# Performance work log

Hardware: AMD Instinct MI355X
Metric: run time of the kernel (lower is better)

Reference implementation:

```python
import jax, jax.numpy as jnp
import numpy as np

SW, SH = 240.0, 180.0  # sensor size from LIFSpikePool(..., (240, 180))
EPS = 1e-5


def _grid_edges(gw, gh):
    # static 8-neighbor (king-move) grid graph + self loops, src -> dst
    idx = np.arange(gw * gh).reshape(gh, gw)
    srcs, dsts = [], []
    for dy in (-1, 0, 1):
        for dx in (-1, 0, 1):
            s = idx[max(0, dy):gh - max(0, -dy), max(0, dx):gw - max(0, -dx)]
            d = idx[max(0, -dy):gh - max(0, dy), max(0, -dx):gw - max(0, dx)]
            srcs.append(s.reshape(-1)); dsts.append(d.reshape(-1))
    return (jnp.asarray(np.concatenate(srcs), jnp.int32),
            jnp.asarray(np.concatenate(dsts), jnp.int32))

_E1 = _grid_edges(80, 60)
_E2 = _grid_edges(40, 30)
_E3 = _grid_edges(20, 15)


def _bn(h):
    # BatchNorm1d with gamma=1, beta=0 (per initialize_weights), batch stats
    return (h - h.mean(0)) / jnp.sqrt(h.var(0) + EPS)


def _pnconv(x, pos2, src, dst, W, b):
    # PointNetConv with single-Linear nn: msg = Lin([x_j, pos_j - pos_i]), max-aggr
    n = x.shape[0]
    msg = jnp.concatenate([x[src], pos2[src] - pos2[dst]], axis=1) @ W + b
    agg = jax.ops.segment_max(msg, dst, num_segments=n)
    return jnp.where(jnp.isfinite(agg), agg, 0.0)  # empty segments -> 0


def _block(x, pos, src, dst, c1w, c1b, c2w, c2b, lw, lb):
    p2 = pos[:, :2]
    skip = _bn(x @ lw + lb)
    h = jax.nn.relu(_bn(_pnconv(x, p2, src, dst, c1w, c1b)))
    h = _bn(_pnconv(h, p2, src, dst, c2w, c2b))
    return jax.nn.relu(h + skip)


def _pool(x, pos, gw, gh, W, b):
    # LIF spike pooling: integrate membrane per grid cell, fire if v > 1
    cx = jnp.clip((pos[:, 0] * gw / SW).astype(jnp.int32), 0, gw - 1)
    cy = jnp.clip((pos[:, 1] * gh / SH).astype(jnp.int32), 0, gh - 1)
    cell = cy * gw + cx
    mem = jax.ops.segment_sum(x, cell, num_segments=gw * gh)
    v = mem @ W + b
    xo = jnp.where(v > 1.0, v, 0.0)
    gx, gy = jnp.meshgrid(jnp.arange(gw), jnp.arange(gh))  # (gh, gw)
    npos = jnp.stack([(gx.reshape(-1) + 0.5) * SW / gw,
                      (gy.reshape(-1) + 0.5) * SH / gh,
                      jnp.zeros(gw * gh)], axis=1).astype(jnp.float32)
    return xo, npos


def _forward(edge_index, x, pos, *p):
    src, dst = edge_index[0], edge_index[1]
    h = _block(x, pos, src, dst, *p[0:6])
    h, pos = _pool(h, pos, 80, 60, p[24], p[25])
    h = _block(h, pos, _E1[0], _E1[1], *p[6:12]); feat0 = h   # (4800, 32)
    h, pos = _pool(h, pos, 40, 30, p[26], p[27])
    h = _block(h, pos, _E2[0], _E2[1], *p[12:18]); feat1 = h  # (1200, 64)
    h, pos = _pool(h, pos, 20, 15, p[28], p[29])
    h = _block(h, pos, _E3[0], _E3[1], *p[18:24]); feat2 = h  # (300, 128)
    return feat0, feat1, feat2


PNAMES = [f"b{i}_{t}" for i in (1, 2, 3, 4) for t in ("c1w", "c1b", "c2w", "c2b", "lw", "lb")] + \
         [f"p{j}_{t}" for j in (1, 2, 3) for t in ("w", "b")]


def setup_inputs() -> dict:
    key = jax.random.key(0)
    ks = jax.random.split(key, 20)
    N, E = 200000, 3200000
    x = jax.random.normal(ks[0], (N, 1), jnp.float32)
    pos = jax.random.uniform(ks[1], (N, 3), jnp.float32) * jnp.array([SW, SH, 1.0], jnp.float32)
    edge_index = jax.random.randint(ks[2], (2, E), 0, N, jnp.int32)
    def lin(k, fi, fo):
        return jax.random.normal(k, (fi, fo), jnp.float32) * np.sqrt(2.0 / fi)
    inp = {"x": x, "pos": pos, "edge_index": edge_index}
    ki = 3
    for i, (ci, co) in enumerate([(1, 16), (16, 32), (32, 64), (64, 128)], start=1):
        inp[f"b{i}_c1w"] = lin(ks[ki], ci + 2, co); ki += 1
        inp[f"b{i}_c1b"] = jnp.zeros((co,), jnp.float32)
        inp[f"b{i}_c2w"] = lin(ks[ki], co + 2, co); ki += 1
        inp[f"b{i}_c2b"] = jnp.zeros((co,), jnp.float32)
        inp[f"b{i}_lw"] = lin(ks[ki], ci, co); ki += 1
        inp[f"b{i}_lb"] = jnp.zeros((co,), jnp.float32)
    for j, ch in [(1, 16), (2, 32), (3, 64)]:
        inp[f"p{j}_w"] = lin(ks[ki], ch, ch); ki += 1
        inp[f"p{j}_b"] = jnp.zeros((ch,), jnp.float32)
    return inp


def reference(x, pos, edge_index,
              b1_c1w, b1_c1b, b1_c2w, b1_c2b, b1_lw, b1_lb,
              b2_c1w, b2_c1b, b2_c2w, b2_c2b, b2_lw, b2_lb,
              b3_c1w, b3_c1b, b3_c2w, b3_c2b, b3_lw, b3_lb,
              b4_c1w, b4_c1b, b4_c2w, b4_c2b, b4_lw, b4_lb,
              p1_w, p1_b, p2_w, p2_b, p3_w, p3_b):
    params = (b1_c1w, b1_c1b, b1_c2w, b1_c2b, b1_lw, b1_lb,
              b2_c1w, b2_c1b, b2_c2w, b2_c2b, b2_lw, b2_lb,
              b3_c1w, b3_c1b, b3_c2w, b3_c2b, b3_lw, b3_lb,
              b4_c1w, b4_c1b, b4_c2w, b4_c2b, b4_lw, b4_lb,
              p1_w, p1_b, p2_w, p2_b, p3_w, p3_b)
    return _forward(edge_index, x, pos, *params)
```

## Files before the change

kernel.cpp:

```cpp
#include <hip/hip_runtime.h>

#define NN 200000
#define NE 3200000
#define NWG 80
#define TT 1024
static constexpr float EPSV = 1e-5f;

__global__ void k_cnt_prep(const int* __restrict__ ei, int* __restrict__ bktCnt,
                           const float* __restrict__ x, const float* __restrict__ pos,
                           float4* __restrict__ feat, float* __restrict__ xstats){
  __shared__ int cnt[256];
  __shared__ float sv[256], sq[256];
  int t = threadIdx.x;
  cnt[t] = 0;
  int i = blockIdx.x*256 + t;
  float xf = 0.f;
  if (i < NN){
    xf = x[i];
    feat[i] = make_float4(xf, pos[3*i], pos[3*i+1], 0.f);
  }
  sv[t] = (i < NN) ? xf : 0.f;
  sq[t] = sv[t]*sv[t];
  __syncthreads();
  int tile = blockIdx.x*4096;
  #pragma unroll
  for (int k = 0; k < 16; ++k){
    int e = tile + k*256 + t;
    if (e < NE) atomicAdd(&cnt[ei[NE+e]>>10], 1);
  }
  for (int o = 128; o > 0; o >>= 1){
    __syncthreads();
    if (t < o){ sv[t]+=sv[t+o]; sq[t]+=sq[t+o]; }
  }
  __syncthreads();
  if (t == 0){ atomicAdd(&xstats[0], sv[0]); atomicAdd(&xstats[1], sq[0]); }
  if (cnt[t]) atomicAdd(&bktCnt[t], cnt[t]);
}

__global__ void k_bktscan(const int* __restrict__ bktCnt, int* __restrict__ bktBase,
                          int* __restrict__ bktCur){
  __shared__ int s[256];
  int t = threadIdx.x;
  int v = bktCnt[t];
  s[t] = v; __syncthreads();
  for (int o = 1; o < 256; o <<= 1){
    int xv = (t >= o) ? s[t-o] : 0;
    __syncthreads(); s[t] += xv; __syncthreads();
  }
  int excl = s[t] - v;
  bktBase[t] = excl;
  bktCur[t]  = excl;
  if (t == 0){ bktBase[256] = NE; }
}

__global__ void k_part1(const int* __restrict__ ei, int* __restrict__ bktCur,
                        int* __restrict__ pairs){
  __shared__ int cnt[256]; __shared__ int base[256]; __shared__ int rank[256];
  int t = threadIdx.x;
  if (t < 256) cnt[t] = 0;
  __syncthreads();
  int tile = blockIdx.x*16384;
  #pragma unroll
  for (int k = 0; k < 16; ++k){
    int e = tile + k*1024 + t;
    if (e < NE) atomicAdd(&cnt[ei[NE+e]>>10], 1);
  }
  __syncthreads();
  if (t < 256){
    base[t] = cnt[t] ? atomicAdd(&bktCur[t], cnt[t]) : 0;
    rank[t] = 0;
  }
  __syncthreads();
  #pragma unroll
  for (int k = 0; k < 16; ++k){
    int e = tile + k*1024 + t;
    if (e < NE){
      int d = ei[NE+e], s = ei[e];
      int b = d >> 10;
      int r = atomicAdd(&rank[b], 1);
      pairs[base[b] + r] = (s<<10) | (d & 1023);
    }
  }
}

__device__ __forceinline__ unsigned fenc(float f){
  unsigned u = __float_as_uint(f);
  return (u >> 31) ? ~u : (u | 0x80000000u);
}
__device__ __forceinline__ float fdec(unsigned k){
  unsigned u = (k >> 31) ? (k ^ 0x80000000u) : ~k;
  return __uint_as_float(u);
}
#define ENC_NI 0x007FFFFFu

__device__ __forceinline__ int aslot(int d, int c){
  return (d << 4) | ((c + (d >> 1)) & 15);
}

__global__ void __launch_bounds__(1024) k_aggA(const int* __restrict__ pairs, const int* __restrict__ bktBase,
    const float4* __restrict__ feat, const float* __restrict__ pos,
    const float* __restrict__ w48, const float* __restrict__ bias,
    float* __restrict__ H, float* __restrict__ st){
  __shared__ unsigned acc[16384];
  const int b = blockIdx.x, t = threadIdx.x;
  for (int i = t; i < 16384; i += 1024) acc[i] = ENC_NI;
  float w0[16], w1[16], w2[16];
  #pragma unroll
  for (int c = 0; c < 16; ++c){ w0[c]=w48[c]; w1[c]=w48[16+c]; w2[c]=w48[32+c]; }
  const int p0 = bktBase[b], p1 = bktBase[b+1];
  __syncthreads();
  for (int j = p0 + t; j < p1; j += 1024){
    int pr = pairs[j];
    float4 f = feat[pr >> 10];
    int d = pr & 1023;
    int gbase = d << 4;
    int rot = (d >> 1) & 15;
    #pragma unroll
    for (int c = 0; c < 16; ++c){
      float m = f.x*w0[c] + f.y*w1[c] + f.z*w2[c];
      atomicMax(&acc[gbase | ((c + rot) & 15)], fenc(m));
    }
  }
  __syncthreads();
  const int base = b << 10;
  const int width = min(1024, NN - base);
  const int c = t & 15;
  const float b_c = bias[c], w1c = w48[16+c], w2c = w48[32+c];
  float ls = 0.f, lq = 0.f;
  for (int i = t; i < width*16; i += 1024){
    int dl = i >> 4, d = base + dl;
    int rot = (dl >> 1) & 15;
    float o = 0.f;
    if (acc[(dl << 4) | rot] != ENC_NI){
      float px = pos[3*d], py = pos[3*d+1];
      o = fdec(acc[(dl << 4) | ((c + rot) & 15)]) + b_c - (px*w1c + py*w2c);
    }
    H[base*16 + i] = o;
    ls += o; lq += o*o;
  }
  __syncthreads();
  float* sv = (float*)acc; float* sq = sv + 1024;
  sv[t] = ls; sq[t] = lq; __syncthreads();
  for (int o2 = 512; o2 >= 16; o2 >>= 1){ if (t < o2){ sv[t]+=sv[t+o2]; sq[t]+=sq[t+o2]; } __syncthreads(); }
  if (t < 16){ atomicAdd(&st[t], sv[t]); atomicAdd(&st[16+t], sq[t]); }
}

__global__ void __launch_bounds__(1024) k_aggB(const int* __restrict__ pairs, const int* __restrict__ bktBase,
    const float4* __restrict__ A4, const float* __restrict__ pos,
    const float* __restrict__ wpos, const float* __restrict__ bias,
    float* __restrict__ H, float* __restrict__ st){
  __shared__ unsigned acc[16384];
  const int b = blockIdx.x, t = threadIdx.x;
  for (int i = t; i < 16384; i += 1024) acc[i] = ENC_NI;
  const int p0 = bktBase[b], p1 = bktBase[b+1];
  __syncthreads();
  for (int j = p0 + t; j < p1; j += 1024){
    int pr = pairs[j];
    int s = pr >> 10;
    int d = pr & 1023;
    int gbase = d << 4;
    int rot = (d >> 1) & 15;
    float4 a0 = A4[s*4+0], a1 = A4[s*4+1], a2 = A4[s*4+2], a3 = A4[s*4+3];
    float av[16] = {a0.x,a0.y,a0.z,a0.w, a1.x,a1.y,a1.z,a1.w,
                    a2.x,a2.y,a2.z,a2.w, a3.x,a3.y,a3.z,a3.w};
    #pragma unroll
    for (int c = 0; c < 16; ++c)
      atomicMax(&acc[gbase | ((c + rot) & 15)], fenc(av[c]));
  }
  __syncthreads();
  const int base = b << 10;
  const int width = min(1024, NN - base);
  const int c = t & 15;
  const float b_c = bias[c], w1c = wpos[c], w2c = wpos[16+c];
  float ls = 0.f, lq = 0.f;
  for (int i = t; i < width*16; i += 1024){
    int dl = i >> 4, d = base + dl;
    int rot = (dl >> 1) & 15;
    float o = 0.f;
    if (acc[(dl << 4) | rot] != ENC_NI){
      float px = pos[3*d], py = pos[3*d+1];
      o = fdec(acc[(dl << 4) | ((c + rot) & 15)]) + b_c - (px*w1c + py*w2c);
    }
    H[base*16 + i] = o;
    ls += o; lq += o*o;
  }
  __syncthreads();
  float* sv = (float*)acc; float* sq = sv + 1024;
  sv[t] = ls; sq[t] = lq; __syncthreads();
  for (int o2 = 512; o2 >= 16; o2 >>= 1){ if (t < o2){ sv[t]+=sv[t+o2]; sq[t]+=sq[t+o2]; } __syncthreads(); }
  if (t < 16){ atomicAdd(&st[t], sv[t]); atomicAdd(&st[16+t], sq[t]); }
}

__global__ void k_prep2(const float* __restrict__ Hraw, const float* __restrict__ st1,
                        const float* __restrict__ pos, const float* __restrict__ w,
                        float4* __restrict__ A4){
  int idx = blockIdx.x*blockDim.x + threadIdx.x;
  if (idx >= NN*4) return;
  int i = idx >> 2, cg = idx & 3;
  const float inv_n = 1.f/(float)NN;
  float acc0 = 0.f, acc1 = 0.f, acc2 = 0.f, acc3 = 0.f;
  #pragma unroll
  for (int k = 0; k < 16; ++k){
    float mk = st1[k]*inv_n;
    float vk = st1[16+k]*inv_n - mk*mk;
    float ik = rsqrtf(vk + EPSV);
    float h = fmaxf((Hraw[i*16+k]-mk)*ik, 0.f);
    acc0 += h*w[k*16 + cg*4 + 0];
    acc1 += h*w[k*16 + cg*4 + 1];
    acc2 += h*w[k*16 + cg*4 + 2];
    acc3 += h*w[k*16 + cg*4 + 3];
  }
  float px = pos[3*i], py = pos[3*i+1];
  int c0 = cg*4;
  acc0 += px*w[256+c0+0] + py*w[272+c0+0];
  acc1 += px*w[256+c0+1] + py*w[272+c0+1];
  acc2 += px*w[256+c0+2] + py*w[272+c0+2];
  acc3 += px*w[256+c0+3] + py*w[272+c0+3];
  A4[idx] = make_float4(acc0, acc1, acc2, acc3);
}

__global__ void k_comb_pool(const float* __restrict__ H, const float* __restrict__ x,
                            const float* __restrict__ pos, const float* __restrict__ lw,
                            const float* __restrict__ st2, const float* __restrict__ xstats,
                            float* __restrict__ mem){
  int idx = blockIdx.x*blockDim.x + threadIdx.x;
  if (idx >= NN*4) return;
  int i = idx >> 2, cg = idx & 3;
  const float inv_n = 1.f/(float)NN;
  float mx = xstats[0]*inv_n, vx = xstats[1]*inv_n - mx*mx;
  float xc = x[i] - mx;
  float px = pos[3*i], py = pos[3*i+1];
  int cx = (int)(px * 80.f / 240.f); cx = min(max(cx,0),79);
  int cy = (int)(py * 60.f / 180.f); cy = min(max(cy,0),59);
  float* mrow = &mem[(cy*80+cx)*16 + cg*4];
  #pragma unroll
  for (int k = 0; k < 4; ++k){
    int c = cg*4 + k;
    float m2 = st2[c]*inv_n, v2 = st2[16+c]*inv_n - m2*m2;
    float i2 = rsqrtf(v2 + EPSV);
    float a = lw[c];
    float sc = a * rsqrtf(a*a*vx + EPSV);
    float v = (H[i*16+c]-m2)*i2 + xc*sc;
    v = fmaxf(v, 0.f);
    atomicAdd(&mrow[k], v);
  }
}

__device__ __forceinline__ void stwt(float* p, float v){
  __hip_atomic_store(p, v, __ATOMIC_RELAXED, __HIP_MEMORY_SCOPE_AGENT);
}
__device__ __forceinline__ float ldwt(const float* p){
  return __hip_atomic_load(p, __ATOMIC_RELAXED, __HIP_MEMORY_SCOPE_AGENT);
}

__device__ __forceinline__ void gridbar(int* bar, int target){
  __syncthreads();
  const int t = threadIdx.x;
  if (blockIdx.x == 0){
    if (t >= 1 && t < NWG){
      while (__hip_atomic_load(bar + 32*t, __ATOMIC_RELAXED, __HIP_MEMORY_SCOPE_AGENT) < target)
        __builtin_amdgcn_s_sleep(1);
    }
    __syncthreads();
    if (t == 0)
      __hip_atomic_store(bar + 2560, target, __ATOMIC_RELAXED, __HIP_MEMORY_SCOPE_AGENT);
  } else {
    if (t == 0){
      __atomic_signal_fence(__ATOMIC_SEQ_CST);
      __builtin_amdgcn_s_waitcnt(0);
      __atomic_signal_fence(__ATOMIC_SEQ_CST);
      __hip_atomic_store(bar + 32*blockIdx.x, target, __ATOMIC_RELAXED, __HIP_MEMORY_SCOPE_AGENT);
      while (__hip_atomic_load(bar + 2560, __ATOMIC_RELAXED, __HIP_MEMORY_SCOPE_AGENT) < target)
        __builtin_amdgcn_s_sleep(2);
    }
    __syncthreads();
  }
}

struct TailP {
  const float *mem1;
  const float *p1w,*p1b,*p2w,*p2b,*p3w,*p3b;
  const float *c1w2,*c1b2,*c2w2,*c2b2,*lw2,*lb2;
  const float *c1w3,*c1b3,*c2w3,*c2b3,*lw3,*lb3;
  const float *c1w4,*c1b4,*c2w4,*c2b4,*lw4,*lb4;
  float *g2p,*g3p;
  float *stB2sk,*stB2c1,*stB2c2,*stB3sk,*stB3c1,*stB3c2,*stB4sk,*stB4c1,*stB4c2;
  float *out;
  int *bar;
};

template<int GW,int GH,int TW,int TH,int K,int C,bool FIRST>
__device__ __forceinline__ void ph_A(float* buf, float* sv, float* sq,
    const float* __restrict__ Gglob, const float* __restrict__ plw, const float* __restrict__ plb,
    const float* __restrict__ c1w, const float* __restrict__ c1b,
    const float* __restrict__ lw, const float* __restrict__ lb,
    float* stH1, float* stSK, float sx, float sy, int tile)
{
  constexpr int W2=TW+4, nR2=W2*(TH+4);
  constexpr int W1=TW+2, nR1=W1*(TH+2);
  constexpr int nT=TW*TH, NTX=GW/TW;
  const int tx0=(tile%NTX)*TW, ty0=(tile/NTX)*TH;
  float* Gl=buf; float* Sl=Gl+nR2*K; float* H1l=Sl+nR2*C; float* SKl=H1l+nR1*C;
  const int t=threadIdx.x;
  if constexpr (FIRST){
    for (int e=t; e<nR2*K; e+=TT){
      int cell=e/K, k=e-cell*K;
      int gx=tx0-2+cell%W2, gy=ty0-2+cell/W2;
      Sl[e] = (gx>=0&&gx<GW&&gy>=0&&gy<GH) ? Gglob[(gy*GW+gx)*K+k] : 0.f;
    }
    __syncthreads();
    for (int e=t; e<nR2*K; e+=TT){
      int cell=e/K, c=e-cell*K;
      float acc=plb[c];
      #pragma unroll
      for (int k=0;k<K;++k) acc += Sl[cell*K+k]*plw[k*K+c];
      Gl[e] = (acc>1.f)?acc:0.f;
    }
  } else {
    for (int e=t; e<nR2*K; e+=TT){
      int cell=e/K, k=e-cell*K;
      int gx=tx0-2+cell%W2, gy=ty0-2+cell/W2;
      Gl[e] = (gx>=0&&gx<GW&&gy>=0&&gy<GH) ? ldwt(&Gglob[(gy*GW+gx)*K+k]) : 0.f;
    }
  }
  __syncthreads();
  for (int e=t; e<nR2*C; e+=TT){
    int cell=e/C, c=e-cell*C;
    float acc=0.f;
    #pragma unroll 8
    for (int k=0;k<K;++k) acc += Gl[cell*K+k]*c1w[k*C+c];
    Sl[e]=acc;
  }
  float ls=0.f,lq=0.f;
  for (int e=t; e<nT*C; e+=TT){
    int cell=e/C, c=e-cell*C;
    int lx=cell%TW, ly=cell/TW;
    int g2=(ly+2)*W2+(lx+2);
    float acc=lb[c];
    #pragma unroll 8
    for (int k=0;k<K;++k) acc += Gl[g2*K+k]*lw[k*C+c];
    SKl[e]=acc; ls+=acc; lq+=acc*acc;
  }
  __syncthreads();
  sv[t]=ls; sq[t]=lq; __syncthreads();
  for (int o=TT/2;o>=C;o>>=1){ if(t<o){sv[t]+=sv[t+o];sq[t]+=sq[t+o];} __syncthreads(); }
  if (t<C){ atomicAdd(&stSK[t],sv[t]); atomicAdd(&stSK[C+t],sq[t]); }
  __syncthreads();
  ls=0.f; lq=0.f;
  const float NI=-__builtin_inff();
  for (int e=t; e<nR1*C; e+=TT){
    int cell=e/C, c=e-cell*C;
    int lx=cell%W1, ly=cell/W1;
    int gx=tx0-1+lx, gy=ty0-1+ly;
    if (gx<0||gx>=GW||gy<0||gy>=GH) continue;
    float wx=c1w[K*C+c], wy=c1w[(K+1)*C+c];
    float m=NI;
    #pragma unroll
    for (int oy=-1;oy<=1;++oy){
// ... 66 lines not shown
      for (int ox=-1;ox<=1;++ox){
        int nx=gx+ox; if (nx<0||nx>=GW) continue;
        int l1=(ly+1+oy)*W1+(lx+1+ox);
        m=fmaxf(m, Sl[l1*C+c]+(ox*sx)*wx+(oy*sy)*wy);
      }
    }
    float val=m+c2b[c];
    H2l[e]=val; ls+=val; lq+=val*val;
  }
  __syncthreads();
  sv[t]=ls; sq[t]=lq; __syncthreads();
  for (int o=TT/2;o>=C;o>>=1){ if(t<o){sv[t]+=sv[t+o];sq[t]+=sq[t+o];} __syncthreads(); }
  if (t<C){ atomicAdd(&stH2[t],sv[t]); atomicAdd(&stH2[C+t],sq[t]); }
}

template<int GW,int GH,int TW,int TH,int K,int C,bool POOL>
__device__ __forceinline__ void ph_C(float* buf, float* asv, float* asq, float* la, float* lbv,
    const float* stH2, const float* stSK,
    const float* __restrict__ pw, const float* __restrict__ pb,
    float* __restrict__ outg, float* __restrict__ Gpg, int tile)
{
  constexpr int W2=TW+4, nR2=W2*(TH+4);
  constexpr int W1=TW+2, nR1=W1*(TH+2);
  constexpr int nT=TW*TH, NTX=GW/TW;
  const int tx0=(tile%NTX)*TW, ty0=(tile/NTX)*TH;
  float* Gl=buf; float* Sl=Gl+nR2*K; float* H1l=Sl+nR2*C; float* SKl=H1l+nR1*C; float* H2l=SKl+nT*C;
  const int t=threadIdx.x;
  const float invn=1.f/(float)(GW*GH);
  if (t<C){
    float m2=ldwt(&stH2[t])*invn, v2=ldwt(&stH2[C+t])*invn-m2*m2;
    float i2=rsqrtf(v2+EPSV);
    la[t]=i2; lbv[t]=-m2*i2;
    float ms=ldwt(&stSK[t])*invn, vs=ldwt(&stSK[C+t])*invn-ms*ms;
    float is_=rsqrtf(vs+EPSV);
    asv[t]=is_; asq[t]=-ms*is_;
  }
  __syncthreads();
  float* OUTl=Sl;
  for (int e=t;e<nT*C;e+=TT){
    int cell=e/C,c=e-cell*C;
    int lx=cell%TW, ly=cell/TW;
    int gx=tx0+lx, gy=ty0+ly;
    float v=(H2l[e]*la[c]+lbv[c])+(SKl[e]*asv[c]+asq[c]);
    v=fmaxf(v,0.f);
    outg[(gy*GW+gx)*C+c]=v;
    OUTl[e]=v;
  }
  if constexpr (POOL){
    __syncthreads();
    constexpr int PTW=TW/2, PTH=TH/2, nP=PTW*PTH, PGW=GW/2;
    float* Ml=H1l;
    for (int e=t;e<nP*C;e+=TT){
      int pc=e/C,c=e-pc*C;
      int plx=pc%PTW, ply=pc/PTW;
      float s=0.f;
      #pragma unroll
      for (int dy=0;dy<2;++dy)
        #pragma unroll
        for (int dx=0;dx<2;++dx)
          s += OUTl[((2*ply+dy)*TW+(2*plx+dx))*C+c];
      Ml[e]=s;
    }
    __syncthreads();
    for (int e=t;e<nP*C;e+=TT){
      int pc=e/C,c=e-pc*C;
      int plx=pc%PTW, ply=pc/PTW;
      float acc=pb[c];
      #pragma unroll 8
      for (int k=0;k<C;++k) acc += Ml[pc*C+k]*pw[k*C+c];
      int gpx=tx0/2+plx, gpy=ty0/2+ply;
      stwt(&Gpg[(gpy*PGW+gpx)*C+c], (acc>1.f)?acc:0.f);
    }
  }
  (void)nR1;
}

__global__ void __launch_bounds__(TT) k_tail(TailP P){
  __shared__ float sv[TT], sq[TT], la[128], lbv[128];
  __shared__ float buf[13824];
  int* bar = P.bar;
  const int tile = blockIdx.x;

  if (tile < 80) ph_A<80,60,10,6,16,32,true >(buf,sv,sq,P.mem1,P.p1w,P.p1b,P.c1w2,P.c1b2,P.lw2,P.lb2,P.stB2c1,P.stB2sk,3.f,3.f,tile);
  gridbar(bar, 1);
  if (tile < 80) ph_B<80,60,10,6,16,32>(buf,sv,sq,la,lbv,P.c2w2,P.c2b2,P.stB2c1,P.stB2c2,3.f,3.f,tile);
  gridbar(bar, 2);
  if (tile < 80) ph_C<80,60,10,6,16,32,true >(buf,sv,sq,la,lbv,P.stB2c2,P.stB2sk,P.p2w,P.p2b,P.out,P.g2p,tile);
  gridbar(bar, 3);
  if (tile < 50) ph_A<40,30,4,6,32,64,false>(buf,sv,sq,P.g2p,nullptr,nullptr,P.c1w3,P.c1b3,P.lw3,P.lb3,P.stB3c1,P.stB3sk,6.f,6.f,tile);
  gridbar(bar, 4);
  if (tile < 50) ph_B<40,30,4,6,32,64>(buf,sv,sq,la,lbv,P.c2w3,P.c2b3,P.stB3c1,P.stB3c2,6.f,6.f,tile);
  gridbar(bar, 5);
  if (tile < 50) ph_C<40,30,4,6,32,64,true >(buf,sv,sq,la,lbv,P.stB3c2,P.stB3sk,P.p3w,P.p3b,P.out+153600,P.g3p,tile);
  gridbar(bar, 6);
  if (tile < 50) ph_A<20,15,2,3,64,128,false>(buf,sv,sq,P.g3p,nullptr,nullptr,P.c1w4,P.c1b4,P.lw4,P.lb4,P.stB4c1,P.stB4sk,12.f,12.f,tile);
  gridbar(bar, 7);
  if (tile < 50) ph_B<20,15,2,3,64,128>(buf,sv,sq,la,lbv,P.c2w4,P.c2b4,P.stB4c1,P.stB4c2,12.f,12.f,tile);
  gridbar(bar, 8);
  if (tile < 50) ph_C<20,15,2,3,64,128,false>(buf,sv,sq,la,lbv,P.stB4c2,P.stB4sk,nullptr,nullptr,P.out+230400,nullptr,tile);
}

extern "C" void kernel_launch(void* const* d_in, const int* in_sizes, int n_in,
                              void* d_out, int out_size, void* d_ws, size_t ws_size,
                              hipStream_t stream){
  const float* x   = (const float*)d_in[0];
  const float* pos = (const float*)d_in[1];
  const int*   ei  = (const int*)d_in[2];
  const float* b1_c1w = (const float*)d_in[3];
  const float* b1_c1b = (const float*)d_in[4];
  const float* b1_c2w = (const float*)d_in[5];
  const float* b1_c2b = (const float*)d_in[6];
  const float* b1_lw  = (const float*)d_in[7];
  const float* b2_c1w = (const float*)d_in[9];
  const float* b2_c1b = (const float*)d_in[10];
  const float* b2_c2w = (const float*)d_in[11];
  const float* b2_c2b = (const float*)d_in[12];
  const float* b2_lw  = (const float*)d_in[13];
  const float* b2_lb  = (const float*)d_in[14];
  const float* b3_c1w = (const float*)d_in[15];
  const float* b3_c1b = (const float*)d_in[16];
  const float* b3_c2w = (const float*)d_in[17];
  const float* b3_c2b = (const float*)d_in[18];
  const float* b3_lw  = (const float*)d_in[19];
  const float* b3_lb  = (const float*)d_in[20];
  const float* b4_c1w = (const float*)d_in[21];
  const float* b4_c1b = (const float*)d_in[22];
  const float* b4_c2w = (const float*)d_in[23];
  const float* b4_c2b = (const float*)d_in[24];
  const float* b4_lw  = (const float*)d_in[25];
  const float* b4_lb  = (const float*)d_in[26];
  const float* p1w = (const float*)d_in[27];
  const float* p1b = (const float*)d_in[28];
  const float* p2w = (const float*)d_in[29];
  const float* p2b = (const float*)d_in[30];
  const float* p3w = (const float*)d_in[31];
  const float* p3b = (const float*)d_in[32];
  float* out = (float*)d_out;

  float4* feat = (float4*)d_ws;
  float* A  = (float*)(feat + NN);
  float* g2p  = A;
  float* g3p  = A + 38400;
  float* H  = A + NN*16;
  int* bktCnt  = (int*)(H + NN*16);
  int* bktBase = bktCnt + 256;
  int* bktCur  = bktBase + 257;
  int* bar     = bktCnt + 1024;
  float* STz   = (float*)(bktCnt + 1024 + 2624);
  float* xstats = STz;
  float* st1    = STz + 16;
  float* st2    = STz + 64;
  float* stB2sk = STz + 128;
  float* stB2c1 = STz + 192;
  float* stB2c2 = STz + 256;
  float* stB3sk = STz + 320;
  float* stB3c1 = STz + 448;
  float* stB3c2 = STz + 576;
  float* stB4sk = STz + 704;
  float* stB4c1 = STz + 960;
  float* stB4c2 = STz + 1216;
  float* mem1   = STz + 1536;
  const size_t ZBYTES = (size_t)(1024 + 2624 + 1536 + 76800) * 4;
  int* pairs  = (int*)(mem1 + 76800);

  hipMemsetAsync(bktCnt, 0, ZBYTES, stream);

  const int B = 256;
  k_cnt_prep<<<(NE+4095)/4096, 256, 0, stream>>>(ei, bktCnt, x, pos, feat, xstats);
  k_bktscan <<<1, 256, 0, stream>>>(bktCnt, bktBase, bktCur);
  k_part1   <<<(NE+16383)/16384, 1024, 0, stream>>>(ei, bktCur, pairs);

  k_aggA    <<<196, 1024, 0, stream>>>(pairs, bktBase, feat, pos, b1_c1w, b1_c1b, H, st1);
  k_prep2   <<<(NN*4+B-1)/B, B, 0, stream>>>(H, st1, pos, b1_c2w, (float4*)A);
  k_aggB    <<<196, 1024, 0, stream>>>(pairs, bktBase, (const float4*)A, pos, b1_c2w+256, b1_c2b, H, st2);
  k_comb_pool<<<(NN*4+B-1)/B, B, 0, stream>>>(H, x, pos, b1_lw, st2, xstats, mem1);

  TailP P;
  P.mem1 = mem1;
  P.p1w = p1w; P.p1b = p1b; P.p2w = p2w; P.p2b = p2b; P.p3w = p3w; P.p3b = p3b;
  P.c1w2 = b2_c1w; P.c1b2 = b2_c1b; P.c2w2 = b2_c2w; P.c2b2 = b2_c2b; P.lw2 = b2_lw; P.lb2 = b2_lb;
  P.c1w3 = b3_c1w; P.c1b3 = b3_c1b; P.c2w3 = b3_c2w; P.c2b3 = b3_c2b; P.lw3 = b3_lw; P.lb3 = b3_lb;
  P.c1w4 = b4_c1w; P.c1b4 = b4_c1b; P.c2w4 = b4_c2w; P.c2b4 = b4_c2b; P.lw4 = b4_lw; P.lb4 = b4_lb;
  P.g2p = g2p; P.g3p = g3p;
  P.stB2sk = stB2sk; P.stB2c1 = stB2c1; P.stB2c2 = stB2c2;
  P.stB3sk = stB3sk; P.stB3c1 = stB3c1; P.stB3c2 = stB3c2;
  P.stB4sk = stB4sk; P.stB4c1 = stB4c1; P.stB4c2 = stB4c2;
  P.out = out; P.bar = bar;
  k_tail<<<NWG, TT, 0, stream>>>(P);
}
```

Measured before the change: 430.2 us.

## Replace global-atomic pooling with LDS-privatized partial histograms and reduction pass

The first LIF pooling stage previously did one global float atomicAdd per node-channel into the 4800x16 membrane grid. It now runs 64 workgroups, each taking a 4-channel group and a 12500-node slice, accumulating into a padded shared-memory copy of the grid, then writing partials that a second small kernel sums. This removes global atomic contention on hot cells, but adds an extra launch, a partials buffer of about 4.9 MB, and uses only 64 workgroups for the main pass.

```diff
diff --git a/kernel.cpp b/kernel.cpp
--- a/kernel.cpp
+++ b/kernel.cpp
@@ -92,10 +92,6 @@
   return __uint_as_float(u);
 }
 #define ENC_NI 0x007FFFFFu
-
-__device__ __forceinline__ int aslot(int d, int c){
-  return (d << 4) | ((c + (d >> 1)) & 15);
-}
 
 __global__ void __launch_bounds__(1024) k_aggA(const int* __restrict__ pairs, const int* __restrict__ bktBase,
     const float4* __restrict__ feat, const float* __restrict__ pos,
@@ -219,31 +215,62 @@
   A4[idx] = make_float4(acc0, acc1, acc2, acc3);
 }
 
-__global__ void k_comb_pool(const float* __restrict__ H, const float* __restrict__ x,
-                            const float* __restrict__ pos, const float* __restrict__ lw,
-                            const float* __restrict__ st2, const float* __restrict__ xstats,
-                            float* __restrict__ mem){
-  int idx = blockIdx.x*blockDim.x + threadIdx.x;
-  if (idx >= NN*4) return;
-  int i = idx >> 2, cg = idx & 3;
+__global__ void __launch_bounds__(1024) k_pool1(const float* __restrict__ H, const float* __restrict__ x,
+    const float* __restrict__ pos, const float* __restrict__ lw,
+    const float* __restrict__ st2, const float* __restrict__ xstats,
+    float* __restrict__ partials){
+  __shared__ float lmem[24000];
+  const int wgid = blockIdx.x;
+  const int g = wgid & 3;
+  const int w = wgid >> 2;
+  const int t = threadIdx.x;
+  for (int i = t; i < 24000; i += 1024) lmem[i] = 0.f;
   const float inv_n = 1.f/(float)NN;
-  float mx = xstats[0]*inv_n, vx = xstats[1]*inv_n - mx*mx;
-  float xc = x[i] - mx;
-  float px = pos[3*i], py = pos[3*i+1];
-  int cx = (int)(px * 80.f / 240.f); cx = min(max(cx,0),79);
-  int cy = (int)(py * 60.f / 180.f); cy = min(max(cy,0),59);
-  float* mrow = &mem[(cy*80+cx)*16 + cg*4];
+  const float mx = xstats[0]*inv_n, vx = xstats[1]*inv_n - mx*mx;
+  const int c0 = g*4;
+  float m2[4], i2[4], sc[4];
   #pragma unroll
   for (int k = 0; k < 4; ++k){
-    int c = cg*4 + k;
-    float m2 = st2[c]*inv_n, v2 = st2[16+c]*inv_n - m2*m2;
-    float i2 = rsqrtf(v2 + EPSV);
+    int c = c0+k;
+    float m = st2[c]*inv_n, v = st2[16+c]*inv_n - m*m;
+    m2[k] = m; i2[k] = rsqrtf(v + EPSV);
     float a = lw[c];
-    float sc = a * rsqrtf(a*a*vx + EPSV);
-    float v = (H[i*16+c]-m2)*i2 + xc*sc;
-    v = fmaxf(v, 0.f);
-    atomicAdd(&mrow[k], v);
-  }
+    sc[k] = a * rsqrtf(a*a*vx + EPSV);
+  }
+  __syncthreads();
+  const int n0 = w*12500, n1 = n0 + 12500;
+  for (int n = n0 + t; n < n1; n += 1024){
+    float4 h4 = *reinterpret_cast<const float4*>(&H[n*16 + c0]);
+    float hv[4] = {h4.x, h4.y, h4.z, h4.w};
+    float xc = x[n] - mx;
+    float px = pos[3*n], py = pos[3*n+1];
+    int cx = (int)(px * 80.f / 240.f); cx = min(max(cx,0),79);
+    int cy = (int)(py * 60.f / 180.f); cy = min(max(cy,0),59);
+    int cb = (cy*80+cx)*5;
+    #pragma unroll
+    for (int k = 0; k < 4; ++k){
+      float v = (hv[k]-m2[k])*i2[k] + xc*sc[k];
+      atomicAdd(&lmem[cb+k], fmaxf(v, 0.f));
+    }
+  }
+  __syncthreads();
+  float* dst = partials + wgid*19200;
+  for (int i = t; i < 19200; i += 1024){
+    int cell = i >> 2, k = i & 3;
+    dst[i] = lmem[cell*5 + k];
+  }
+}
+
+__global__ void k_pool2(const float* __restrict__ partials, float* __restrict__ mem){
+  int idx = blockIdx.x*256 + threadIdx.x;
+  if (idx >= 76800) return;
+  int cell = idx >> 4, c = idx & 15;
+  int g = c >> 2, k = c & 3;
+  float s = 0.f;
+  #pragma unroll
+  for (int w = 0; w < 16; ++w)
+    s += partials[(w*4 + g)*19200 + cell*4 + k];
+  mem[idx] = s;
 }
 
 __device__ __forceinline__ void stwt(float* p, float v){
@@ -565,6 +592,7 @@
   float* A  = (float*)(feat + NN);
   float* g2p  = A;
   float* g3p  = A + 38400;
+  float* partials = A + 65536;
   float* H  = A + NN*16;
   int* bktCnt  = (int*)(H + NN*16);
   int* bktBase = bktCnt + 256;
@@ -597,7 +625,9 @@
   k_aggA    <<<196, 1024, 0, stream>>>(pairs, bktBase, feat, pos, b1_c1w, b1_c1b, H, st1);
   k_prep2   <<<(NN*4+B-1)/B, B, 0, stream>>>(H, st1, pos, b1_c2w, (float4*)A);
   k_aggB    <<<196, 1024, 0, stream>>>(pairs, bktBase, (const float4*)A, pos, b1_c2w+256, b1_c2b, H, st2);
-  k_comb_pool<<<(NN*4+B-1)/B, B, 0, stream>>>(H, x, pos, b1_lw, st2, xstats, mem1);
+
+  k_pool1   <<<64, 1024, 0, stream>>>(H, x, pos, b1_lw, st2, xstats, partials);
+  k_pool2   <<<300, 256, 0, stream>>>(partials, mem1);
 
   TailP P;
   P.mem1 = mem1;
```

New measurement: 453.3 us. 1.05x slower.

## Fuse block-1 scan, partition, aggregation and BN into persistent grid-barrier kernels

Applied to the files above, without the earlier changes.

Merges bucket scan, edge partition, first conv aggregation and the BN+linear prep into one persistent kernel synchronized with software grid barriers. The second aggregation now keeps its max accumulator in LDS across a grid barrier and applies BN, skip and pooling directly, so the H intermediate is never written to or read from global memory. BN statistics go to 16 striped partial slots to reduce atomic contention. The costs are that all 196 workgroups of 1024 threads must be co-resident or the barrier deadlocks, and the max aggregation is recomputed from LDS in two passes.

```diff
diff --git a/kernel.cpp b/kernel.cpp
--- a/kernel.cpp
+++ b/kernel.cpp
@@ -3,8 +3,46 @@
 #define NN 200000
 #define NE 3200000
 #define NWG 80
+#define NBKT 196
 #define TT 1024
 static constexpr float EPSV = 1e-5f;
+
+__device__ __forceinline__ void stwt(float* p, float v){
+  __hip_atomic_store(p, v, __ATOMIC_RELAXED, __HIP_MEMORY_SCOPE_AGENT);
+}
+__device__ __forceinline__ float ldwt(const float* p){
+  return __hip_atomic_load(p, __ATOMIC_RELAXED, __HIP_MEMORY_SCOPE_AGENT);
+}
+__device__ __forceinline__ void stwt_i(int* p, int v){
+  __hip_atomic_store(p, v, __ATOMIC_RELAXED, __HIP_MEMORY_SCOPE_AGENT);
+}
+__device__ __forceinline__ int ldwt_i(const int* p){
+  return __hip_atomic_load(p, __ATOMIC_RELAXED, __HIP_MEMORY_SCOPE_AGENT);
+}
+
+__device__ __forceinline__ void gridbar(int* bar, int target, int nwg){
+  __syncthreads();
+  const int t = threadIdx.x;
+  if (blockIdx.x == 0){
+    if (t >= 1 && t < nwg){
+      while (__hip_atomic_load(bar + 32*t, __ATOMIC_RELAXED, __HIP_MEMORY_SCOPE_AGENT) < target)
+        __builtin_amdgcn_s_sleep(1);
+    }
+    __syncthreads();
+    if (t == 0)
+      __hip_atomic_store(bar + 6272, target, __ATOMIC_RELAXED, __HIP_MEMORY_SCOPE_AGENT);
+  } else {
+    if (t == 0){
+      __atomic_signal_fence(__ATOMIC_SEQ_CST);
+      __builtin_amdgcn_s_waitcnt(0);
+      __atomic_signal_fence(__ATOMIC_SEQ_CST);
+      __hip_atomic_store(bar + 32*blockIdx.x, target, __ATOMIC_RELAXED, __HIP_MEMORY_SCOPE_AGENT);
+      while (__hip_atomic_load(bar + 6272, __ATOMIC_RELAXED, __HIP_MEMORY_SCOPE_AGENT) < target)
+        __builtin_amdgcn_s_sleep(2);
+    }
+    __syncthreads();
+  }
+}
 
 __global__ void k_cnt_prep(const int* __restrict__ ei, int* __restrict__ bktCnt,
                            const float* __restrict__ x, const float* __restrict__ pos,
@@ -37,52 +75,6 @@
   if (cnt[t]) atomicAdd(&bktCnt[t], cnt[t]);
 }
 
-__global__ void k_bktscan(const int* __restrict__ bktCnt, int* __restrict__ bktBase,
-                          int* __restrict__ bktCur){
-  __shared__ int s[256];
-  int t = threadIdx.x;
-  int v = bktCnt[t];
-  s[t] = v; __syncthreads();
-  for (int o = 1; o < 256; o <<= 1){
-    int xv = (t >= o) ? s[t-o] : 0;
-    __syncthreads(); s[t] += xv; __syncthreads();
-  }
-  int excl = s[t] - v;
-  bktBase[t] = excl;
-  bktCur[t]  = excl;
-  if (t == 0){ bktBase[256] = NE; }
-}
-
-__global__ void k_part1(const int* __restrict__ ei, int* __restrict__ bktCur,
-                        int* __restrict__ pairs){
-  __shared__ int cnt[256]; __shared__ int base[256]; __shared__ int rank[256];
-  int t = threadIdx.x;
-  if (t < 256) cnt[t] = 0;
-  __syncthreads();
-  int tile = blockIdx.x*16384;
-  #pragma unroll
-  for (int k = 0; k < 16; ++k){
-    int e = tile + k*1024 + t;
-    if (e < NE) atomicAdd(&cnt[ei[NE+e]>>10], 1);
-  }
-  __syncthreads();
-  if (t < 256){
-    base[t] = cnt[t] ? atomicAdd(&bktCur[t], cnt[t]) : 0;
-    rank[t] = 0;
-  }
-  __syncthreads();
-  #pragma unroll
-  for (int k = 0; k < 16; ++k){
-    int e = tile + k*1024 + t;
-    if (e < NE){
-      int d = ei[NE+e], s = ei[e];
-      int b = d >> 10;
-      int r = atomicAdd(&rank[b], 1);
-      pairs[base[b] + r] = (s<<10) | (d & 1023);
-    }
-  }
-}
-
 __device__ __forceinline__ unsigned fenc(float f){
   unsigned u = __float_as_uint(f);
   return (u >> 31) ? ~u : (u | 0x80000000u);
@@ -93,187 +85,223 @@
 }
 #define ENC_NI 0x007FFFFFu
 
-__device__ __forceinline__ int aslot(int d, int c){
-  return (d << 4) | ((c + (d >> 1)) & 15);
-}
-
-__global__ void __launch_bounds__(1024) k_aggA(const int* __restrict__ pairs, const int* __restrict__ bktBase,
-    const float4* __restrict__ feat, const float* __restrict__ pos,
-    const float* __restrict__ w48, const float* __restrict__ bias,
-    float* __restrict__ H, float* __restrict__ st){
+__global__ void __launch_bounds__(1024) k_b1(const int* __restrict__ ei,
+    const int* __restrict__ bktCnt, int* __restrict__ bktBase, int* __restrict__ bktCur,
+    int* __restrict__ pairs, const float4* __restrict__ feat, const float* __restrict__ pos,
+    const float* __restrict__ w48, const float* __restrict__ biasA,
+    const float* __restrict__ w2, float* __restrict__ st1p, float4* __restrict__ A4,
+    int* __restrict__ bar){
   __shared__ unsigned acc[16384];
-  const int b = blockIdx.x, t = threadIdx.x;
+  const int t = threadIdx.x, wg = blockIdx.x;
+
+  if (wg == 0){
+    int* s = (int*)acc;
+    int v = 0;
+    if (t < 256){ v = ldwt_i(&bktCnt[t]); s[t] = v; }
+    __syncthreads();
+    for (int o = 1; o < 256; o <<= 1){
+      int xv = 0;
+      if (t >= o && t < 256) xv = s[t-o];
+      __syncthreads();
+      if (t < 256) s[t] += xv;
+      __syncthreads();
+    }
+    if (t < 256){ stwt_i(&bktBase[t], s[t]-v); stwt_i(&bktCur[t], s[t]-v); }
+    if (t == 0) stwt_i(&bktBase[256], NE);
+  }
+  gridbar(bar, 1, NBKT);
+
+  {
+    int* cnt = (int*)acc; int* base = cnt + 256; int* rank = base + 256;
+    if (t < 256) cnt[t] = 0;
+    __syncthreads();
+    int tile = wg*16384;
+    #pragma unroll
+    for (int k = 0; k < 16; ++k){
+      int e = tile + k*1024 + t;
+      if (e < NE) atomicAdd(&cnt[ei[NE+e]>>10], 1);
+    }
+    __syncthreads();
+    if (t < 256){
+      base[t] = cnt[t] ? atomicAdd(&bktCur[t], cnt[t]) : 0;
+      rank[t] = 0;
+    }
+    __syncthreads();
+    #pragma unroll
+    for (int k = 0; k < 16; ++k){
+      int e = tile + k*1024 + t;
+      if (e < NE){
+        int d = ei[NE+e], ssrc = ei[e];
+        int b = d >> 10;
+        int r = atomicAdd(&rank[b], 1);
+        stwt_i(&pairs[base[b] + r], (ssrc<<10) | (d & 1023));
+      }
+    }
+  }
+  gridbar(bar, 2, NBKT);
+
   for (int i = t; i < 16384; i += 1024) acc[i] = ENC_NI;
-  float w0[16], w1[16], w2[16];
+  float wa0[16], wa1[16], wa2[16];
   #pragma unroll
-  for (int c = 0; c < 16; ++c){ w0[c]=w48[c]; w1[c]=w48[16+c]; w2[c]=w48[32+c]; }
-  const int p0 = bktBase[b], p1 = bktBase[b+1];
+  for (int c = 0; c < 16; ++c){ wa0[c]=w48[c]; wa1[c]=w48[16+c]; wa2[c]=w48[32+c]; }
+  const int p0 = ldwt_i(&bktBase[wg]), p1 = ldwt_i(&bktBase[wg+1]);
+  __syncthreads();
+  for (int j = p0 + t; j < p1; j += 1024){
+    int pr = ldwt_i(&pairs[j]);
+    float4 f = feat[pr >> 10];
+    int d = pr & 1023;
+    int gb = d << 4, rot = (d >> 1) & 15;
+    #pragma unroll
+    for (int c = 0; c < 16; ++c){
+      float m = f.x*wa0[c] + f.y*wa1[c] + f.z*wa2[c];
+      atomicMax(&acc[gb | ((c + rot) & 15)], fenc(m));
+    }
+  }
+  __syncthreads();
+  const int base = wg << 10;
+  const int width = min(1024, NN - base);
+  {
+    const int c = t & 15;
+    const float b_c = biasA[c], w1c = w48[16+c], w2c = w48[32+c];
+    float ls = 0.f, lq = 0.f;
+    for (int i = t; i < width*16; i += 1024){
+      int dl = i >> 4, d = base + dl;
+      int rot = (dl >> 1) & 15;
+      float o = 0.f;
+      if (acc[(dl<<4) | rot] != ENC_NI){
+        float px = pos[3*d], py = pos[3*d+1];
+        o = fdec(acc[(dl<<4) | ((c + rot) & 15)]) + b_c - (px*w1c + py*w2c);
+      }
+      ls += o; lq += o*o;
+    }
+    ls += __shfl_xor(ls, 16, 64); ls += __shfl_xor(ls, 32, 64);
+    lq += __shfl_xor(lq, 16, 64); lq += __shfl_xor(lq, 32, 64);
+    if ((t & 63) < 16){
+      int slot = (wg + (t >> 6)) & 15;
+      atomicAdd(&st1p[slot*32 + c], ls);
+      atomicAdd(&st1p[slot*32 + 16 + c], lq);
+    }
+  }
+  gridbar(bar, 3, NBKT);
+
+  {
+    const int lane = t & 63;
+    float stv = 0.f;
+    if (lane < 32){
+      #pragma unroll
+      for (int s2 = 0; s2 < 16; ++s2) stv += ldwt(&st1p[s2*32 + lane]);
+    }
+    const float inv_n = 1.f/(float)NN;
+    float mk[16], ik[16];
+    #pragma unroll
+    for (int k = 0; k < 16; ++k){
+      float sm = __shfl(stv, k, 64);
+      float sq_ = __shfl(stv, 16 + k, 64);
+      float m = sm*inv_n;
+      float v = sq_*inv_n - m*m;
+      mk[k] = m; ik[k] = rsqrtf(v + EPSV);
+    }
+    for (int i = t; i < width*4; i += 1024){
+      int dl = i >> 2, cg = i & 3, d = base + dl;
+      int rot = (dl >> 1) & 15;
+      bool valid = (acc[(dl<<4) | rot] != ENC_NI);
+      float px = pos[3*d], py = pos[3*d+1];
+      float a0=0.f,a1=0.f,a2=0.f,a3=0.f;
+      #pragma unroll
+      for (int k = 0; k < 16; ++k){
+        float o = 0.f;
+        if (valid) o = fdec(acc[(dl<<4) | ((k + rot) & 15)]) + biasA[k] - (px*w48[16+k] + py*w48[32+k]);
+        float h = fmaxf((o - mk[k])*ik[k], 0.f);
+        a0 += h*w2[k*16 + cg*4 + 0];
+        a1 += h*w2[k*16 + cg*4 + 1];
+        a2 += h*w2[k*16 + cg*4 + 2];
+        a3 += h*w2[k*16 + cg*4 + 3];
+      }
+      int c0 = cg*4;
+      a0 += px*w2[256+c0+0] + py*w2[272+c0+0];
+      a1 += px*w2[256+c0+1] + py*w2[272+c0+1];
+      a2 += px*w2[256+c0+2] + py*w2[272+c0+2];
+      a3 += px*w2[256+c0+3] + py*w2[272+c0+3];
+      A4[d*4 + cg] = make_float4(a0,a1,a2,a3);
+    }
+  }
+}
+
+__global__ void __launch_bounds__(1024) k_aggBC(const int* __restrict__ pairs, const int* __restrict__ bktBase,
+    const float4* __restrict__ A4, const float* __restrict__ pos, const float* __restrict__ x,
+    const float* __restrict__ wpos, const float* __restrict__ biasB, const float* __restrict__ lw,
+    float* __restrict__ st2p, const float* __restrict__ xstats,
+    float* __restrict__ mem1, int* __restrict__ bar){
+  __shared__ unsigned acc[16384];
+  const int t = threadIdx.x, wg = blockIdx.x;
+  for (int i = t; i < 16384; i += 1024) acc[i] = ENC_NI;
+  const int p0 = bktBase[wg], p1 = bktBase[wg+1];
   __syncthreads();
   for (int j = p0 + t; j < p1; j += 1024){
     int pr = pairs[j];
-    float4 f = feat[pr >> 10];
-    int d = pr & 1023;
-    int gbase = d << 4;
-    int rot = (d >> 1) & 15;
-    #pragma unroll
-    for (int c = 0; c < 16; ++c){
-      float m = f.x*w0[c] + f.y*w1[c] + f.z*w2[c];
-      atomicMax(&acc[gbase | ((c + rot) & 15)], fenc(m));
-    }
-  }
-  __syncthreads();
-  const int base = b << 10;
-  const int width = min(1024, NN - base);
-  const int c = t & 15;
-  const float b_c = bias[c], w1c = w48[16+c], w2c = w48[32+c];
-  float ls = 0.f, lq = 0.f;
-  for (int i = t; i < width*16; i += 1024){
-    int dl = i >> 4, d = base + dl;
-    int rot = (dl >> 1) & 15;
-    float o = 0.f;
-    if (acc[(dl << 4) | rot] != ENC_NI){
-      float px = pos[3*d], py = pos[3*d+1];
-      o = fdec(acc[(dl << 4) | ((c + rot) & 15)]) + b_c - (px*w1c + py*w2c);
-    }
-    H[base*16 + i] = o;
-    ls += o; lq += o*o;
-  }
-  __syncthreads();
-  float* sv = (float*)acc; float* sq = sv + 1024;
-  sv[t] = ls; sq[t] = lq; __syncthreads();
-  for (int o2 = 512; o2 >= 16; o2 >>= 1){ if (t < o2){ sv[t]+=sv[t+o2]; sq[t]+=sq[t+o2]; } __syncthreads(); }
-  if (t < 16){ atomicAdd(&st[t], sv[t]); atomicAdd(&st[16+t], sq[t]); }
-}
-
-__global__ void __launch_bounds__(1024) k_aggB(const int* __restrict__ pairs, const int* __restrict__ bktBase,
-    const float4* __restrict__ A4, const float* __restrict__ pos,
-    const float* __restrict__ wpos, const float* __restrict__ bias,
-    float* __restrict__ H, float* __restrict__ st){
-  __shared__ unsigned acc[16384];
-  const int b = blockIdx.x, t = threadIdx.x;
-  for (int i = t; i < 16384; i += 1024) acc[i] = ENC_NI;
-  const int p0 = bktBase[b], p1 = bktBase[b+1];
-  __syncthreads();
-  for (int j = p0 + t; j < p1; j += 1024){
-    int pr = pairs[j];
-    int s = pr >> 10;
-    int d = pr & 1023;
-    int gbase = d << 4;
-    int rot = (d >> 1) & 15;
+    int s = pr >> 10, d = pr & 1023;
+    int gb = d << 4, rot = (d >> 1) & 15;
     float4 a0 = A4[s*4+0], a1 = A4[s*4+1], a2 = A4[s*4+2], a3 = A4[s*4+3];
     float av[16] = {a0.x,a0.y,a0.z,a0.w, a1.x,a1.y,a1.z,a1.w,
                     a2.x,a2.y,a2.z,a2.w, a3.x,a3.y,a3.z,a3.w};
     #pragma unroll
     for (int c = 0; c < 16; ++c)
-      atomicMax(&acc[gbase | ((c + rot) & 15)], fenc(av[c]));
-  }
-  __syncthreads();
-  const int base = b << 10;
+      atomicMax(&acc[gb | ((c + rot) & 15)], fenc(av[c]));
+  }
+  __syncthreads();
+  const int base = wg << 10;
   const int width = min(1024, NN - base);
   const int c = t & 15;
-  const float b_c = bias[c], w1c = wpos[c], w2c = wpos[16+c];
-  float ls = 0.f, lq = 0.f;
-  for (int i = t; i < width*16; i += 1024){
-    int dl = i >> 4, d = base + dl;
-    int rot = (dl >> 1) & 15;
-    float o = 0.f;
-    if (acc[(dl << 4) | rot] != ENC_NI){
-      float px = pos[3*d], py = pos[3*d+1];
-      o = fdec(acc[(dl << 4) | ((c + rot) & 15)]) + b_c - (px*w1c + py*w2c);
-    }
-    H[base*16 + i] = o;
-    ls += o; lq += o*o;
-  }
-  __syncthreads();
-  float* sv = (float*)acc; float* sq = sv + 1024;
-  sv[t] = ls; sq[t] = lq; __syncthreads();
-  for (int o2 = 512; o2 >= 16; o2 >>= 1){ if (t < o2){ sv[t]+=sv[t+o2]; sq[t]+=sq[t+o2]; } __syncthreads(); }
-  if (t < 16){ atomicAdd(&st[t], sv[t]); atomicAdd(&st[16+t], sq[t]); }
-}
-
-__global__ void k_prep2(const float* __restrict__ Hraw, const float* __restrict__ st1,
-                        const float* __restrict__ pos, const float* __restrict__ w,
-                        float4* __restrict__ A4){
-  int idx = blockIdx.x*blockDim.x + threadIdx.x;
-  if (idx >= NN*4) return;
-  int i = idx >> 2, cg = idx & 3;
-  const float inv_n = 1.f/(float)NN;
-  float acc0 = 0.f, acc1 = 0.f, acc2 = 0.f, acc3 = 0.f;
-  #pragma unroll
-  for (int k = 0; k < 16; ++k){
-    float mk = st1[k]*inv_n;
-    float vk = st1[16+k]*inv_n - mk*mk;
-    float ik = rsqrtf(vk + EPSV);
-    float h = fmaxf((Hraw[i*16+k]-mk)*ik, 0.f);
-    acc0 += h*w[k*16 + cg*4 + 0];
-    acc1 += h*w[k*16 + cg*4 + 1];
-    acc2 += h*w[k*16 + cg*4 + 2];
-    acc3 += h*w[k*16 + cg*4 + 3];
-  }
-  float px = pos[3*i], py = pos[3*i+1];
-  int c0 = cg*4;
-  acc0 += px*w[256+c0+0] + py*w[272+c0+0];
-  acc1 += px*w[256+c0+1] + py*w[272+c0+1];
-  acc2 += px*w[256+c0+2] + py*w[272+c0+2];
-  acc3 += px*w[256+c0+3] + py*w[272+c0+3];
-  A4[idx] = make_float4(acc0, acc1, acc2, acc3);
-}
-
-__global__ void k_comb_pool(const float* __restrict__ H, const float* __restrict__ x,
-                            const float* __restrict__ pos, const float* __restrict__ lw,
-                            const float* __restrict__ st2, const float* __restrict__ xstats,
-                            float* __restrict__ mem){
-  int idx = blockIdx.x*blockDim.x + threadIdx.x;
-  if (idx >= NN*4) return;
-  int i = idx >> 2, cg = idx & 3;
-  const float inv_n = 1.f/(float)NN;
-  float mx = xstats[0]*inv_n, vx = xstats[1]*inv_n - mx*mx;
-  float xc = x[i] - mx;
-  float px = pos[3*i], py = pos[3*i+1];
-  int cx = (int)(px * 80.f / 240.f); cx = min(max(cx,0),79);
-  int cy = (int)(py * 60.f / 180.f); cy = min(max(cy,0),59);
-  float* mrow = &mem[(cy*80+cx)*16 + cg*4];
-  #pragma unroll
-  for (int k = 0; k < 4; ++k){
-    int c = cg*4 + k;
-    float m2 = st2[c]*inv_n, v2 = st2[16+c]*inv_n - m2*m2;
+  const float b_c = biasB[c], w1c = wpos[c], w2c = wpos[16+c];
+  {
+    float ls = 0.f, lq = 0.f;
+    for (int i = t; i < width*16; i += 1024){
+      int dl = i >> 4, d = base + dl;
+      int rot = (dl >> 1) & 15;
+      float o = 0.f;
+      if (acc[(dl<<4) | rot] != ENC_NI){
+        float px = pos[3*d], py = pos[3*d+1];
+        o = fdec(acc[(dl<<4) | ((c + rot) & 15)]) + b_c - (px*w1c + py*w2c);
+      }
+      ls += o; lq += o*o;
+    }
+    ls += __shfl_xor(ls, 16, 64); ls += __shfl_xor(ls, 32, 64);
+    lq += __shfl_xor(lq, 16, 64); lq += __shfl_xor(lq, 32, 64);
+    if ((t & 63) < 16){
+      int slot = (wg + (t >> 6)) & 15;
+      atomicAdd(&st2p[slot*32 + c], ls);
+      atomicAdd(&st2p[slot*32 + 16 + c], lq);
+    }
+  }
+  gridbar(bar, 4, NBKT);
+  {
+    const int lane = t & 63;
+    float stv = 0.f;
+    if (lane < 32){
+      #pragma unroll
+      for (int s2 = 0; s2 < 16; ++s2) stv += ldwt(&st2p[s2*32 + lane]);
+    }
+    const float inv_n = 1.f/(float)NN;
+    float sm = __shfl(stv, c, 64), sq_ = __shfl(stv, 16 + c, 64);
+    float m2 = sm*inv_n, v2 = sq_*inv_n - m2*m2;
     float i2 = rsqrtf(v2 + EPSV);
+    float mx = ldwt(&xstats[0])*inv_n;
+    float vx = ldwt(&xstats[1])*inv_n - mx*mx;
     float a = lw[c];
     float sc = a * rsqrtf(a*a*vx + EPSV);
-    float v = (H[i*16+c]-m2)*i2 + xc*sc;
-    v = fmaxf(v, 0.f);
-    atomicAdd(&mrow[k], v);
-  }
-}
-
-__device__ __forceinline__ void stwt(float* p, float v){
-  __hip_atomic_store(p, v, __ATOMIC_RELAXED, __HIP_MEMORY_SCOPE_AGENT);
-}
-__device__ __forceinline__ float ldwt(const float* p){
-  return __hip_atomic_load(p, __ATOMIC_RELAXED, __HIP_MEMORY_SCOPE_AGENT);
-}
-
-__device__ __forceinline__ void gridbar(int* bar, int target){
-  __syncthreads();
-  const int t = threadIdx.x;
-  if (blockIdx.x == 0){
-    if (t >= 1 && t < NWG){
-      while (__hip_atomic_load(bar + 32*t, __ATOMIC_RELAXED, __HIP_MEMORY_SCOPE_AGENT) < target)
-        __builtin_amdgcn_s_sleep(1);
-    }
-    __syncthreads();
-    if (t == 0)
-      __hip_atomic_store(bar + 2560, target, __ATOMIC_RELAXED, __HIP_MEMORY_SCOPE_AGENT);
-  } else {
-    if (t == 0){
-      __atomic_signal_fence(__ATOMIC_SEQ_CST);
-      __builtin_amdgcn_s_waitcnt(0);
-      __atomic_signal_fence(__ATOMIC_SEQ_CST);
-      __hip_atomic_store(bar + 32*blockIdx.x, target, __ATOMIC_RELAXED, __HIP_MEMORY_SCOPE_AGENT);
-      while (__hip_atomic_load(bar + 2560, __ATOMIC_RELAXED, __HIP_MEMORY_SCOPE_AGENT) < target)
-        __builtin_amdgcn_s_sleep(2);
-    }
-    __syncthreads();
+    for (int i = t; i < width*16; i += 1024){
+      int dl = i >> 4, d = base + dl;
+      int rot = (dl >> 1) & 15;
+      float px = pos[3*d], py = pos[3*d+1];
+      float o = 0.f;
+      if (acc[(dl<<4) | rot] != ENC_NI)
+        o = fdec(acc[(dl<<4) | ((c + rot) & 15)]) + b_c - (px*w1c + py*w2c);
+      float v = (o - m2)*i2 + (x[d]-mx)*sc;
+      v = fmaxf(v, 0.f);
+      int cx = (int)(px * 80.f / 240.f); cx = min(max(cx,0),79);
+      int cy = (int)(py * 60.f / 180.f); cy = min(max(cy,0),59);
+      atomicAdd(&mem1[(cy*80+cx)*16 + c], v);
+    }
   }
 }
 
@@ -506,21 +534,21 @@
   const int tile = blockIdx.x;
 
   if (tile < 80) ph_A<80,60,10,6,16,32,true >(buf,sv,sq,P.mem1,P.p1w,P.p1b,P.c1w2,P.c1b2,P.lw2,P.lb2,P.stB2c1,P.stB2sk,3.f,3.f,tile);
-  gridbar(bar, 1);
+  gridbar(bar, 5, NWG);
   if (tile < 80) ph_B<80,60,10,6,16,32>(buf,sv,sq,la,lbv,P.c2w2,P.c2b2,P.stB2c1,P.stB2c2,3.f,3.f,tile);
-  gridbar(bar, 2);
+  gridbar(bar, 6, NWG);
   if (tile < 80) ph_C<80,60,10,6,16,32,true >(buf,sv,sq,la,lbv,P.stB2c2,P.stB2sk,P.p2w,P.p2b,P.out,P.g2p,tile);
-  gridbar(bar, 3);
+  gridbar(bar, 7, NWG);
   if (tile < 50) ph_A<40,30,4,6,32,64,false>(buf,sv,sq,P.g2p,nullptr,nullptr,P.c1w3,P.c1b3,P.lw3,P.lb3,P.stB3c1,P.stB3sk,6.f,6.f,tile);
-  gridbar(bar, 4);
+  gridbar(bar, 8, NWG);
   if (tile < 50) ph_B<40,30,4,6,32,64>(buf,sv,sq,la,lbv,P.c2w3,P.c2b3,P.stB3c1,P.stB3c2,6.f,6.f,tile);
-  gridbar(bar, 5);
+  gridbar(bar, 9, NWG);
   if (tile < 50) ph_C<40,30,4,6,32,64,true >(buf,sv,sq,la,lbv,P.stB3c2,P.stB3sk,P.p3w,P.p3b,P.out+153600,P.g3p,tile);
-  gridbar(bar, 6);
+  gridbar(bar, 10, NWG);
   if (tile < 50) ph_A<20,15,2,3,64,128,false>(buf,sv,sq,P.g3p,nullptr,nullptr,P.c1w4,P.c1b4,P.lw4,P.lb4,P.stB4c1,P.stB4sk,12.f,12.f,tile);
-  gridbar(bar, 7);
+  gridbar(bar, 11, NWG);
   if (tile < 50) ph_B<20,15,2,3,64,128>(buf,sv,sq,la,lbv,P.c2w4,P.c2b4,P.stB4c1,P.stB4c2,12.f,12.f,tile);
-  gridbar(bar, 8);
+  gridbar(bar, 12, NWG);
   if (tile < 50) ph_C<20,15,2,3,64,128,false>(buf,sv,sq,la,lbv,P.stB4c2,P.stB4sk,nullptr,nullptr,P.out+230400,nullptr,tile);
 }
 
@@ -565,39 +593,34 @@
   float* A  = (float*)(feat + NN);
   float* g2p  = A;
   float* g3p  = A + 38400;
-  float* H  = A + NN*16;
-  int* bktCnt  = (int*)(H + NN*16);
+  int* bktCnt  = (int*)(A + NN*16);
   int* bktBase = bktCnt + 256;
   int* bktCur  = bktBase + 257;
   int* bar     = bktCnt + 1024;
-  float* STz   = (float*)(bktCnt + 1024 + 2624);
+  float* STz   = (float*)(bktCnt + 1024 + 6400);
   float* xstats = STz;
-  float* st1    = STz + 16;
-  float* st2    = STz + 64;
-  float* stB2sk = STz + 128;
-  float* stB2c1 = STz + 192;
-  float* stB2c2 = STz + 256;
-  float* stB3sk = STz + 320;
-  float* stB3c1 = STz + 448;
-  float* stB3c2 = STz + 576;
-  float* stB4sk = STz + 704;
-  float* stB4c1 = STz + 960;
-  float* stB4c2 = STz + 1216;
-  float* mem1   = STz + 1536;
-  const size_t ZBYTES = (size_t)(1024 + 2624 + 1536 + 76800) * 4;
+  float* st1p   = STz + 64;
+  float* st2p   = STz + 576;
+  float* stB2sk = STz + 1088;
+  float* stB2c1 = STz + 1152;
+  float* stB2c2 = STz + 1216;
+  float* stB3sk = STz + 1280;
+  float* stB3c1 = STz + 1408;
+  float* stB3c2 = STz + 1536;
+  float* stB4sk = STz + 1664;
+  float* stB4c1 = STz + 1920;
+  float* stB4c2 = STz + 2176;
+  float* mem1   = STz + 2560;
+  const size_t ZBYTES = (size_t)(1024 + 6400 + 2560 + 76800) * 4;
   int* pairs  = (int*)(mem1 + 76800);
 
   hipMemsetAsync(bktCnt, 0, ZBYTES, stream);
 
-  const int B = 256;
   k_cnt_prep<<<(NE+4095)/4096, 256, 0, stream>>>(ei, bktCnt, x, pos, feat, xstats);
-  k_bktscan <<<1, 256, 0, stream>>>(bktCnt, bktBase, bktCur);
-  k_part1   <<<(NE+16383)/16384, 1024, 0, stream>>>(ei, bktCur, pairs);
-
-  k_aggA    <<<196, 1024, 0, stream>>>(pairs, bktBase, feat, pos, b1_c1w, b1_c1b, H, st1);
-  k_prep2   <<<(NN*4+B-1)/B, B, 0, stream>>>(H, st1, pos, b1_c2w, (float4*)A);
-  k_aggB    <<<196, 1024, 0, stream>>>(pairs, bktBase, (const float4*)A, pos, b1_c2w+256, b1_c2b, H, st2);
-  k_comb_pool<<<(NN*4+B-1)/B, B, 0, stream>>>(H, x, pos, b1_lw, st2, xstats, mem1);
+  k_b1   <<<NBKT, TT, 0, stream>>>(ei, bktCnt, bktBase, bktCur, pairs, feat, pos,
+                                   b1_c1w, b1_c1b, b1_c2w, st1p, (float4*)A, bar);
+  k_aggBC<<<NBKT, TT, 0, stream>>>(pairs, bktBase, (const float4*)A, pos, x,
+                                   b1_c2w+256, b1_c2b, b1_lw, st2p, xstats, mem1, bar);
 
   TailP P;
   P.mem1 = mem1;
```

Result: slower. 447.9 us (+4.1%).
